# Performance work log

Hardware: AMD Instinct MI355X
Metric: run time of the kernel (lower is better)

Reference implementation:

```python
import jax, jax.numpy as jnp
import numpy as np

N_NODES = 40000
N_EDGES = 640000
D_IN, D_HID, D_OUT = 128, 128, 40


def _gcn_layer(x, src, dst, norm, W, b, n):
    # PyG GCNConv: h = x @ W; aggregate norm * h[src] at dst; add bias.
    h = x @ W
    msg = norm[:, None] * h[src]          # [E+N, d] gathered messages
    return jax.ops.segment_sum(msg, dst, num_segments=n) + b


def setup_inputs() -> dict:
    key = jax.random.key(0)
    ks = jax.random.split(key, 8)
    x = jax.random.normal(ks[0], (N_NODES, D_IN), dtype=jnp.float32)
    edge_index = jax.random.randint(ks[1], (2, N_EDGES), 0, N_NODES)
    s_in = 1.0 / np.sqrt(D_IN)
    s_hid = 1.0 / np.sqrt(D_HID)
    W1 = jax.random.normal(ks[2], (D_IN, D_HID), dtype=jnp.float32) * s_in
    b1 = jnp.zeros((D_HID,), dtype=jnp.float32)
    W2 = jax.random.normal(ks[3], (D_HID, D_HID), dtype=jnp.float32) * s_hid
    b2 = jnp.zeros((D_HID,), dtype=jnp.float32)
    W3 = jax.random.normal(ks[4], (D_HID, D_OUT), dtype=jnp.float32) * s_hid
    b3 = jnp.zeros((D_OUT,), dtype=jnp.float32)
    return {"x": x, "edge_index": edge_index, "W1": W1, "b1": b1,
            "W2": W2, "b2": b2, "W3": W3, "b3": b3}


def reference(x, edge_index, W1, b1, W2, b2, W3, b3):
    n = x.shape[0]
    src = edge_index[0].astype(jnp.int32)
    dst = edge_index[1].astype(jnp.int32)

    # --- GCN normalization with self-loops (PyG GCNConv defaults) ---
    loops = jnp.arange(n, dtype=jnp.int32)
    src2 = jnp.concatenate([src, loops])
    dst2 = jnp.concatenate([dst, loops])
    deg = jax.ops.segment_sum(jnp.ones_like(dst2, dtype=x.dtype), dst2,
                              num_segments=n)
    dis = jnp.where(deg > 0, jax.lax.rsqrt(deg), 0.0)
    norm = dis[src2] * dis[dst2]          # [E+N]

    h = jax.nn.relu(_gcn_layer(x, src2, dst2, norm, W1, b1, n))
    h = jax.nn.relu(_gcn_layer(h, src2, dst2, norm, W2, b2, n))
    out = _gcn_layer(h, src2, dst2, norm, W3, b3, n)

    # --- reg_loss = trace(A @ A), A = dense COO adjacency (dupes summed) ---
    # trace(A@A) = sum_{i,j} A[i,j] * A[j,i]
    #            = sum over edge instances (i,j) of multiplicity of (j,i).
    # Computed sparsely via sorted key lookup instead of NxN densification.
    keys = src * n + dst                  # unique int32 key per (i,j)
    skeys = jnp.sort(keys)
    rev = dst * n + src
    lo = jnp.searchsorted(skeys, rev, side="left")
    hi = jnp.searchsorted(skeys, rev, side="right")
    reg_loss = jnp.sum((hi - lo).astype(jnp.float32))

    return jax.nn.log_softmax(out, axis=1), reg_loss
```

## Files before the change

### kernel.cpp

```cpp
#include <hip/hip_runtime.h>
#include <hip/hip_bf16.h>
#include <math.h>

#define NN 40000
#define EE 640000
#define CAP 64
#define MPAD 40064
#define LDS_STRIDE 136
#define FP8_STRIDE 144
#define G_STRIDE 72
#define E4B 625

typedef short bf16x8 __attribute__((ext_vector_type(8)));
typedef float f32x16 __attribute__((ext_vector_type(16)));
typedef float f32x2 __attribute__((ext_vector_type(2)));

__device__ __forceinline__ unsigned bf16rne(float x) {
  unsigned u = __float_as_uint(x);
  return (u + 0x7fffu + ((u >> 16) & 1u)) >> 16;
}
__device__ __forceinline__ unsigned packbf2(float lo, float hi) {
  return bf16rne(lo) | (bf16rne(hi) << 16);
}
__device__ __forceinline__ float bflo(unsigned u) {
  return __uint_as_float(u << 16);
}
__device__ __forceinline__ float bfhi(unsigned u) {
  return __uint_as_float(u & 0xffff0000u);
}
__device__ __forceinline__ float dis_of(const int* cnt, int i) {
  return rsqrtf((float)(cnt[i] + 1));
}
__device__ __forceinline__ f32x2 cvt2lo(unsigned u) {
  return __builtin_amdgcn_cvt_pk_f32_fp8((int)u, false);
}
__device__ __forceinline__ f32x2 cvt2hi(unsigned u) {
  return __builtin_amdgcn_cvt_pk_f32_fp8((int)u, true);
}
__device__ __forceinline__ unsigned char f32_to_fp8(float x) {
  return (unsigned char)(__builtin_amdgcn_cvt_pk_fp8_f32(x, x, 0, false) & 0xff);
}

__global__ __launch_bounds__(256) void edge_w_kernel(
    const int4* __restrict__ src4, const int4* __restrict__ dst4,
    int* __restrict__ cnt, unsigned short* __restrict__ csr,
    const float* __restrict__ W1, const float* __restrict__ W2,
    const float* __restrict__ W3, unsigned short* __restrict__ Wt1,
    unsigned short* __restrict__ Wt2, unsigned short* __restrict__ W3t,
    unsigned* __restrict__ Xb32, unsigned* __restrict__ H1b32) {
  int blk = blockIdx.x, t = threadIdx.x;
  if (blk < E4B) {
    int e = blk * 256 + t;
    int4 s = src4[e];
    int4 d = dst4[e];
    int p0 = atomicAdd(&cnt[d.x], 1);
    int p1 = atomicAdd(&cnt[d.y], 1);
    int p2 = atomicAdd(&cnt[d.z], 1);
    int p3 = atomicAdd(&cnt[d.w], 1);
    if (p0 < CAP) csr[d.x * CAP + p0] = (unsigned short)s.x;
    if (p1 < CAP) csr[d.y * CAP + p1] = (unsigned short)s.y;
    if (p2 < CAP) csr[d.z * CAP + p2] = (unsigned short)s.z;
    if (p3 < CAP) csr[d.w * CAP + p3] = (unsigned short)s.w;
  } else if (blk < 753) {
    bool is1 = blk < 689;
    int n = (blk - (is1 ? 625 : 689)) * 2 + (t >> 7);
    int k = t & 127;
    const float* W = is1 ? W1 : W2;
    unsigned short* Wt = is1 ? Wt1 : Wt2;
    Wt[n * 128 + k] = (unsigned short)bf16rne(W[k * 128 + n]);
  } else if (blk < 785) {
    int n = (blk - 753) * 2 + (t >> 7);
    int k = t & 127;
    float v = (n < 40) ? W3[k * 40 + n] : 0.f;
    W3t[n * 128 + k] = (unsigned short)bf16rne(v);
  } else {
    if (t < 32) Xb32[(size_t)NN * 32 + t] = 0u;
    else if (t < 64) H1b32[(size_t)NN * 32 + (t - 32)] = 0u;
  }
}

__global__ __launch_bounds__(256) void fill_x_kernel(
    const int* __restrict__ cnt, const float4* __restrict__ X,
    uint2* __restrict__ Xb8v) {
  int i = blockIdx.x * 256 + threadIdx.x;
  float di = dis_of(cnt, i >> 4);
  float4 a = X[i * 2], b = X[i * 2 + 1];
  int lo = __builtin_amdgcn_cvt_pk_fp8_f32(di * a.x, di * a.y, 0, false);
  lo = __builtin_amdgcn_cvt_pk_fp8_f32(di * a.z, di * a.w, lo, true);
  int hi = __builtin_amdgcn_cvt_pk_fp8_f32(di * b.x, di * b.y, 0, false);
  hi = __builtin_amdgcn_cvt_pk_fp8_f32(di * b.z, di * b.w, hi, true);
  uint2 o;
  o.x = (unsigned)lo;
  o.y = (unsigned)hi;
  Xb8v[i] = o;
}

__device__ __forceinline__ void agg128_body8(
    int node, int sub, const unsigned char* __restrict__ Hb,
    const int* __restrict__ cnt, const unsigned short* __restrict__ csr,
    unsigned* __restrict__ outB) {
  float di = dis_of(cnt, node);
  const unsigned char* Hbs = Hb + sub * 16;
  f32x2 a0, a1, a2, a3, a4, a5, a6, a7;
  {
    uint4 v = *(const uint4*)&Hbs[(size_t)node * 128];
    a0 = cvt2lo(v.x);
    a1 = cvt2hi(v.x);
    a2 = cvt2lo(v.y);
    a3 = cvt2hi(v.y);
    a4 = cvt2lo(v.z);
    a5 = cvt2hi(v.z);
    a6 = cvt2lo(v.w);
    a7 = cvt2hi(v.w);
  }
  int cn = cnt[node];
  cn = cn > CAP ? CAP : cn;
  const unsigned short* row = &csr[node * CAP];
  if (cn > 0) {
    uint4 cs = *(const uint4*)row;
    for (int e = 0; e < cn; e += 8) {
      int rem = cn - e;
      int s0 = cs.x & 0xffff, s1 = cs.x >> 16;
      int s2 = cs.y & 0xffff, s3 = cs.y >> 16;
      int s4 = cs.z & 0xffff, s5 = cs.z >> 16;
      int s6 = cs.w & 0xffff, s7 = cs.w >> 16;
      s1 = rem > 1 ? s1 : NN;
      s2 = rem > 2 ? s2 : NN;
      s3 = rem > 3 ? s3 : NN;
      s4 = rem > 4 ? s4 : NN;
      s5 = rem > 5 ? s5 : NN;
      s6 = rem > 6 ? s6 : NN;
      s7 = rem > 7 ? s7 : NN;
      uint4 v0 = *(const uint4*)&Hbs[(size_t)s0 * 128];
      uint4 v1 = *(const uint4*)&Hbs[(size_t)s1 * 128];
      uint4 v2 = *(const uint4*)&Hbs[(size_t)s2 * 128];
      uint4 v3 = *(const uint4*)&Hbs[(size_t)s3 * 128];
      uint4 v4 = *(const uint4*)&Hbs[(size_t)s4 * 128];
      uint4 v5 = *(const uint4*)&Hbs[(size_t)s5 * 128];
      uint4 v6 = *(const uint4*)&Hbs[(size_t)s6 * 128];
      uint4 v7 = *(const uint4*)&Hbs[(size_t)s7 * 128];
      if (e + 8 < cn) cs = *(const uint4*)&row[e + 8];
#define ACC8(vv)                                    \
  a0 += cvt2lo(vv.x); a1 += cvt2hi(vv.x);           \
  a2 += cvt2lo(vv.y); a3 += cvt2hi(vv.y);           \
  a4 += cvt2lo(vv.z); a5 += cvt2hi(vv.z);           \
  a6 += cvt2lo(vv.w); a7 += cvt2hi(vv.w);
      ACC8(v0);
      ACC8(v1);
      ACC8(v2);
      ACC8(v3);
      ACC8(v4);
      ACC8(v5);
      ACC8(v6);
      ACC8(v7);
#undef ACC8
    }
  }
  unsigned o0 = packbf2(di * a0.x, di * a0.y);
  unsigned o1 = packbf2(di * a1.x, di * a1.y);
  unsigned o2 = packbf2(di * a2.x, di * a2.y);
  unsigned o3 = packbf2(di * a3.x, di * a3.y);
  unsigned o4 = packbf2(di * a4.x, di * a4.y);
  unsigned o5 = packbf2(di * a5.x, di * a5.y);
  unsigned o6 = packbf2(di * a6.x, di * a6.y);
  unsigned o7 = packbf2(di * a7.x, di * a7.y);
  *(uint4*)&outB[(size_t)node * 64 + sub * 8] = make_uint4(o0, o1, o2, o3);
  *(uint4*)&outB[(size_t)node * 64 + sub * 8 + 4] = make_uint4(o4, o5, o6, o7);
}

__global__ __launch_bounds__(256) void agg_reg(
    const unsigned char* __restrict__ Hb8, const int* __restrict__ cnt,
    const unsigned short* __restrict__ csr, unsigned* __restrict__ outB,
    const int* __restrict__ src, const int* __restrict__ dst, int ebase,
    float* __restrict__ out_scalar) {
  int blk = blockIdx.x, t = threadIdx.x;
  if ((blk & 1) == 0) {
    int node = (blk >> 1) * 32 + (t >> 3);
    agg128_body8(node, t & 7, Hb8, cnt, csr, outB);
    return;
  }
  int e = ebase + (blk >> 1) * 256 + t;
  int c = 0;
  {
    int i = src[e];
    unsigned j = (unsigned)dst[e];
    int cn = cnt[i];
    cn = cn > CAP ? CAP : cn;
    const uint4* base = (const uint4*)&csr[i * CAP];
    int full = cn >> 3;
    for (int q = 0; q < full; q++) {
      uint4 v = base[q];
      c += ((v.x & 0xffffu) == j) + ((v.x >> 16) == j);
      c += ((v.y & 0xffffu) == j) + ((v.y >> 16) == j);
      c += ((v.z & 0xffffu) == j) + ((v.z >> 16) == j);
      c += ((v.w & 0xffffu) == j) + ((v.w >> 16) == j);
    }
    int rem = cn & 7;
    if (rem) {
      uint4 v = base[full];
      c += (int)((v.x & 0xffffu) == j);
      c += ((v.x >> 16) == j) & (rem > 1);
      c += ((v.y & 0xffffu) == j) & (rem > 2);
      c += ((v.y >> 16) == j) & (rem > 3);
      c += ((v.z & 0xffffu) == j) & (rem > 4);
      c += ((v.z >> 16) == j) & (rem > 5);
      c += ((v.w & 0xffffu) == j) & (rem > 6);
    }
  }
  float v = (float)c;
  for (int off = 32; off; off >>= 1) v += __shfl_down(v, off, 64);
  __shared__ float ws[4];
  int lane = threadIdx.x & 63, w = threadIdx.x >> 6;
  if (lane == 0) ws[w] = v;
  __syncthreads();
  if (threadIdx.x == 0) atomicAdd(out_scalar, ws[0] + ws[1] + ws[2] + ws[3]);
}

__global__ __launch_bounds__(256) void gemm_mfma(
    const unsigned* __restrict__ Ab, const unsigned* __restrict__ Wt,
    const float* __restrict__ bias, const int* __restrict__ cnt,
    unsigned char* __restrict__ outB8) {
  __shared__ unsigned short At[128 * LDS_STRIDE];
  __shared__ unsigned short Bt[128 * LDS_STRIDE];
  __shared__ float dsh[128];
  int t = threadIdx.x;
  int rowBase = blockIdx.x * 128;
  if (t < 128) {
    int rr = rowBase + t;
    dsh[t] = (rr < NN) ? dis_of(cnt, rr) : 0.f;
  }
  {
    const uint4* ga = (const uint4*)(Ab + (size_t)rowBase * 64);
    const uint4* gw = (const uint4*)Wt;
#pragma unroll
    for (int i = 0; i < 8; i++) {
      int idx = i * 256 + t;
      int r = idx >> 4, c = idx & 15;
      uint4 va = ga[idx];
      uint4 vw = gw[idx];
      *(uint4*)&At[r * LDS_STRIDE + c * 8] = va;
      *(uint4*)&Bt[r * LDS_STRIDE + c * 8] = vw;
    }
  }
  __syncthreads();
  int lane = t & 63, w = t >> 6;
  int m31 = lane & 31;
  int khalf = (lane >> 5) * 8;
  f32x16 acc[4] = {};
#pragma unroll
  for (int ks = 0; ks < 8; ks++) {
    bf16x8 a = *(bf16x8*)&At[(w * 32 + m31) * LDS_STRIDE + ks * 16 + khalf];
#pragma unroll
    for (int nt = 0; nt < 4; nt++) {
      bf16x8 b = *(bf16x8*)&Bt[(nt * 32 + m31) * LDS_STRIDE + ks * 16 + khalf];
      acc[nt] = __builtin_amdgcn_mfma_f32_32x32x16_bf16(a, b, acc[nt], 0, 0, 0);
    }
  }
  __syncthreads();
  unsigned char* Ac = (unsigned char*)At;
  int rsel = (lane >> 5) * 4;
#pragma unroll
  for (int nt = 0; nt < 4; nt++) {
    int col = nt * 32 + m31;
    float bv = bias[col];
#pragma unroll
    for (int r = 0; r < 16; r++) {
      int rl = w * 32 + (r & 3) + 8 * (r >> 2) + rsel;
      float x = fmaxf(acc[nt][r] + bv, 0.f);
      Ac[rl * FP8_STRIDE + col] = f32_to_fp8(dsh[rl] * x);
    }
  }
  __syncthreads();
  {
#pragma unroll
    for (int i = 0; i < 4; i++) {
      int idx = i * 256 + t;
      int r = idx >> 3, c = idx & 7;
      int grow = rowBase + r;
      if (grow < NN) {
        uint4 vv = *(const uint4*)&Ac[r * FP8_STRIDE + c * 16];
        *(uint4*)&outB8[(size_t)grow * 128 + c * 16] = vv;
      }
    }
  }
}

__global__ __launch_bounds__(256) void gemm_mfma2(
    const unsigned* __restrict__ Ab, const unsigned* __restrict__ Wt,
    const float* __restrict__ bias, const int* __restrict__ cnt,
    const unsigned short* __restrict__ W3t, unsigned char* __restrict__ G3b) {
  __shared__ unsigned short At[128 * LDS_STRIDE];
  __shared__ unsigned short Bt[128 * LDS_STRIDE];
  __shared__ float dsh[128];
  int t = threadIdx.x;
  int rowBase = blockIdx.x * 128;
  if (blockIdx.x == 0 && t < 32)
    ((unsigned*)G3b)[(size_t)NN * 32 + t] = 0u;
  if (t < 128) {
    int rr = rowBase + t;
    dsh[t] = (rr < NN) ? dis_of(cnt, rr) : 0.f;
  }
  {
    const uint4* ga = (const uint4*)(Ab + (size_t)rowBase * 64);
    const uint4* gw = (const uint4*)Wt;
#pragma unroll
    for (int i = 0; i < 8; i++) {
      int idx = i * 256 + t;
      int r = idx >> 4, c = idx & 15;
      uint4 va = ga[idx];
      uint4 vw = gw[idx];
      *(uint4*)&At[r * LDS_STRIDE + c * 8] = va;
      *(uint4*)&Bt[r * LDS_STRIDE + c * 8] = vw;
    }
  }
  __syncthreads();
  int lane = t & 63, w = t >> 6;
  int m31 = lane & 31;
  int khalf = (lane >> 5) * 8;
  f32x16 acc[4] = {};
#pragma unroll
  for (int ks = 0; ks < 8; ks++) {
    bf16x8 a = *(bf16x8*)&At[(w * 32 + m31) * LDS_STRIDE + ks * 16 + khalf];
#pragma unroll
    for (int nt = 0; nt < 4; nt++) {
      bf16x8 b = *(bf16x8*)&Bt[(nt * 32 + m31) * LDS_STRIDE + ks * 16 + khalf];
      acc[nt] = __builtin_amdgcn_mfma_f32_32x32x16_bf16(a, b, acc[nt], 0, 0, 0);
    }
  }
  __syncthreads();
  int rsel = (lane >> 5) * 4;
#pragma unroll
  for (int nt = 0; nt < 4; nt++) {
    int col = nt * 32 + m31;
    float bv = bias[col];
#pragma unroll
    for (int r = 0; r < 16; r++) {
      int rl = w * 32 + (r & 3) + 8 * (r >> 2) + rsel;
      float x = fmaxf(acc[nt][r] + bv, 0.f);
      At[rl * LDS_STRIDE + col] = (unsigned short)bf16rne(dsh[rl] * x);
    }
  }
  {
    const uint4* gw3 = (const uint4*)W3t;
#pragma unroll
    for (int i = 0; i < 4; i++) {
      int idx = i * 256 + t;
      int r = idx >> 4, c = idx & 15;
      *(uint4*)&Bt[r * LDS_STRIDE + c * 8] = gw3[idx];
    }
  }
  __syncthreads();
  f32x16 acc2[2] = {};
#pragma unroll
  for (int ks = 0; ks < 8; ks++) {
    bf16x8 a = *(bf16x8*)&At[(w * 32 + m31) * LDS_STRIDE + ks * 16 + khalf];
#pragma unroll
    for (int nt = 0; nt < 2; nt++) {
      bf16x8 b = *(bf16x8*)&Bt[(nt * 32 + m31) * LDS_STRIDE + ks * 16 + khalf];
      acc2[nt] = __builtin_amdgcn_mfma_f32_32x32x16_bf16(a, b, acc2[nt], 0, 0, 0);
    }
  }
  __syncthreads();
  unsigned short* Gs = At;
#pragma unroll
  for (int nt = 0; nt < 2; nt++) {
    int col = nt * 32 + m31;
#pragma unroll
    for (int r = 0; r < 16; r++) {
      int rl = w * 32 + (r & 3) + 8 * (r >> 2) + rsel;
      Gs[rl * G_STRIDE + col] = (unsigned short)bf16rne(acc2[nt][r]);
    }
  }
  __syncthreads();
  {
#pragma unroll
    for (int i = 0; i < 4; i++) {
      int idx = i * 256 + t;
      int r = idx >> 3, c = idx & 7;
      int grow = rowBase + r;
      if (grow < NN) {
        uint4 vv = *(const uint4*)&Gs[r * G_STRIDE + c * 8];
        *(uint4*)&G3b[(size_t)grow * 128 + c * 16] = vv;
      }
    }
  }
}

__global__ __launch_bounds__(256) void agg40b_softmax(
    const unsigned char* __restrict__ Gb, const int* __restrict__ cnt,
    const unsigned short* __restrict__ csr, const float* __restrict__ b3,
    float* __restrict__ outp) {
  int t = threadIdx.x;
  int node = blockIdx.x * 32 + (t >> 3);
  int sub = t & 7;
  const unsigned char* Gs = Gb + sub * 16;
  float di = dis_of(cnt, node);
  float a0, a1, a2, a3, a4, a5, a6, a7;
  {
    uint4 v = *(const uint4*)&Gs[(size_t)node * 128];
    a0 = bflo(v.x); a1 = bfhi(v.x);
    a2 = bflo(v.y); a3 = bfhi(v.y);
    a4 = bflo(v.z); a5 = bfhi(v.z);
    a6 = bflo(v.w); a7 = bfhi(v.w);
  }
  int cn = cnt[node];
  cn = cn > CAP ? CAP : cn;
  const unsigned short* row = &csr[node * CAP];
  if (cn > 0) {
    uint4 cs = *(const uint4*)row;
    for (int e = 0; e < cn; e += 8) {
      int rem = cn - e;
      int s0 = cs.x & 0xffff, s1 = cs.x >> 16;
      int s2 = cs.y & 0xffff, s3 = cs.y >> 16;
      int s4 = cs.z & 0xffff, s5 = cs.z >> 16;
      int s6 = cs.w & 0xffff, s7 = cs.w >> 16;
      s1 = rem > 1 ? s1 : NN;
      s2 = rem > 2 ? s2 : NN;
      s3 = rem > 3 ? s3 : NN;
      s4 = rem > 4 ? s4 : NN;
      s5 = rem > 5 ? s5 : NN;
      s6 = rem > 6 ? s6 : NN;
      s7 = rem > 7 ? s7 : NN;
      uint4 v0 = *(const uint4*)&Gs[(size_t)s0 * 128];
      uint4 v1 = *(const uint4*)&Gs[(size_t)s1 * 128];
      uint4 v2 = *(const uint4*)&Gs[(size_t)s2 * 128];
      uint4 v3 = *(const uint4*)&Gs[(size_t)s3 * 128];
      uint4 v4 = *(const uint4*)&Gs[(size_t)s4 * 128];
      uint4 v5 = *(const uint4*)&Gs[(size_t)s5 * 128];
      uint4 v6 = *(const uint4*)&Gs[(size_t)s6 * 128];
      uint4 v7 = *(const uint4*)&Gs[(size_t)s7 * 128];
      if (e + 8 < cn) cs = *(const uint4*)&row[e + 8];
#define ACCB(vv)                                    \
  a0 += bflo(vv.x); a1 += bfhi(vv.x);               \
  a2 += bflo(vv.y); a3 += bfhi(vv.y);               \
  a4 += bflo(vv.z); a5 += bfhi(vv.z);               \
  a6 += bflo(vv.w); a7 += bfhi(vv.w);
      ACCB(v0);
      ACCB(v1);
      ACCB(v2);
      ACCB(v3);
      ACCB(v4);
      ACCB(v5);
      ACCB(v6);
      ACCB(v7);
#undef ACCB
    }
  }
  bool act = sub < 5;
  int sb = act ? sub : 0;
  const float4* b34 = (const float4*)b3;
  float4 bl = b34[sb * 2], bh = b34[sb * 2 + 1];
  float o0 = di * a0 + bl.x, o1 = di * a1 + bl.y;
  float o2 = di * a2 + bl.z, o3 = di * a3 + bl.w;
  float o4 = di * a4 + bh.x, o5 = di * a5 + bh.y;
  float o6 = di * a6 + bh.z, o7 = di * a7 + bh.w;
  float m = fmaxf(fmaxf(fmaxf(o0, o1), fmaxf(o2, o3)),
                  fmaxf(fmaxf(o4, o5), fmaxf(o6, o7)));
  m = act ? m : -1e30f;
  m = fmaxf(m, __shfl_xor(m, 1, 64));
  m = fmaxf(m, __shfl_xor(m, 2, 64));
  m = fmaxf(m, __shfl_xor(m, 4, 64));
  float s = expf(o0 - m) + expf(o1 - m) + expf(o2 - m) + expf(o3 - m) +
            expf(o4 - m) + expf(o5 - m) + expf(o6 - m) + expf(o7 - m);
  s = act ? s : 0.f;
  s += __shfl_xor(s, 1, 64);
  s += __shfl_xor(s, 2, 64);
  s += __shfl_xor(s, 4, 64);
  float l = m + logf(s);
  if (act) {
    float4 r0, r1;
    r0.x = o0 - l; r0.y = o1 - l; r0.z = o2 - l; r0.w = o3 - l;
    r1.x = o4 - l; r1.y = o5 - l; r1.z = o6 - l; r1.w = o7 - l;
    float* op = &outp[(size_t)node * 40 + sub * 8];
    *(float4*)op = r0;
    *(float4*)(op + 4) = r1;
  }
}

extern "C" void kernel_launch(void* const* d_in, const int* in_sizes, int n_in,
                              void* d_out, int out_size, void* d_ws,
                              size_t ws_size, hipStream_t stream) {
  const float* X = (const float*)d_in[0];
  const int* ei = (const int*)d_in[1];
  const float* W1 = (const float*)d_in[2];
  const float* b1 = (const float*)d_in[3];
  const float* W2 = (const float*)d_in[4];
  const float* b2 = (const float*)d_in[5];
  const float* W3 = (const float*)d_in[6];
  const float* b3 = (const float*)d_in[7];
  float* out = (float*)d_out;

  const int* src = ei;
  const int* dst = ei + EE;

  char* w = (char*)d_ws;
  auto carve = [&](size_t bytes) {
    char* p = w;
    w += (bytes + 255) & ~(size_t)255;
    return p;
  };
  int* cnt = (int*)carve(NN * 4);
  unsigned short* csr = (unsigned short*)carve((size_t)NN * CAP * 2);
  unsigned short* Wt1 = (unsigned short*)carve(128 * 128 * 2);
  unsigned short* Wt2 = (unsigned short*)carve(128 * 128 * 2);
  unsigned short* W3t = (unsigned short*)carve(64 * 128 * 2);
  unsigned* Ab = (unsigned*)carve((size_t)MPAD * 128 * 2);
  char* blk = carve(((size_t)NN + 1) * 128 * 2);
  unsigned char* Xb8 = (unsigned char*)blk;
  unsigned char* H1b8 = (unsigned char*)blk + ((size_t)NN + 1) * 128;
  unsigned char* G3b = (unsigned char*)blk;

  (void)hipMemsetAsync(cnt, 0, NN * 4, stream);
  (void)hipMemsetAsync((char*)d_out + (size_t)NN * 40 * 4, 0, 4, stream);

  const int GB = MPAD / 128;

  edge_w_kernel<<<786, 256, 0, stream>>>((const int4*)src, (const int4*)dst,
                                         cnt, csr, W1, W2, W3, Wt1, Wt2, W3t,
                                         (unsigned*)Xb8, (unsigned*)H1b8);
  fill_x_kernel<<<2500, 256, 0, stream>>>(cnt, (const float4*)X, (uint2*)Xb8);
  agg_reg<<<2500, 256, 0, stream>>>(Xb8, cnt, csr, Ab, src, dst, 0,
                                    out + (size_t)NN * 40);
  gemm_mfma<<<GB, 256, 0, stream>>>(Ab, (const unsigned*)Wt1, b1, cnt, H1b8);
  agg_reg<<<2500, 256, 0, stream>>>(H1b8, cnt, csr, Ab, src, dst, EE / 2,
                                    out + (size_t)NN * 40);
  gemm_mfma2<<<GB, 256, 0, stream>>>(Ab, (const unsigned*)Wt2, b2, cnt, W3t,
                                     G3b);
  agg40b_softmax<<<1250, 256, 0, stream>>>(G3b, cnt, csr, b3, out);
}
```

Before: 194.3 us.

## Split fp8 feature tables into halves and route aggregation work per XCC

Stores the fp8 node-feature tables as two 64-byte column halves, so each aggregation block gathers from only one half. Blocks pick their work through an atomic queue keyed on the XCC id, which steers each half toward a subset of XCDs and keeps its working set in that XCD's L2. CSR loads and bf16 output stores are made nontemporal. This adds per-block atomics and a shared-memory broadcast, and the XCC-to-half mapping depends on hardware dispatch order.

```diff
diff --git a/kernel.cpp b/kernel.cpp
--- a/kernel.cpp
+++ b/kernel.cpp
@@ -14,6 +14,8 @@
 typedef short bf16x8 __attribute__((ext_vector_type(8)));
 typedef float f32x16 __attribute__((ext_vector_type(16)));
 typedef float f32x2 __attribute__((ext_vector_type(2)));
+typedef unsigned u32x4 __attribute__((ext_vector_type(4)));
+typedef unsigned u32x2 __attribute__((ext_vector_type(2)));
 
 __device__ __forceinline__ unsigned bf16rne(float x) {
   unsigned u = __float_as_uint(x);
@@ -47,7 +49,8 @@
     const float* __restrict__ W1, const float* __restrict__ W2,
     const float* __restrict__ W3, unsigned short* __restrict__ Wt1,
     unsigned short* __restrict__ Wt2, unsigned short* __restrict__ W3t,
-    unsigned* __restrict__ Xb32, unsigned* __restrict__ H1b32) {
+    unsigned* __restrict__ XbA32, unsigned* __restrict__ XbB32,
+    unsigned* __restrict__ HA32, unsigned* __restrict__ HB32) {
   int blk = blockIdx.x, t = threadIdx.x;
   if (blk < E4B) {
     int e = blk * 256 + t;
@@ -74,16 +77,19 @@
     float v = (n < 40) ? W3[k * 40 + n] : 0.f;
     W3t[n * 128 + k] = (unsigned short)bf16rne(v);
   } else {
-    if (t < 32) Xb32[(size_t)NN * 32 + t] = 0u;
-    else if (t < 64) H1b32[(size_t)NN * 32 + (t - 32)] = 0u;
+    if (t < 16) XbA32[(size_t)NN * 16 + t] = 0u;
+    else if (t < 32) XbB32[(size_t)NN * 16 + (t - 16)] = 0u;
+    else if (t < 48) HA32[(size_t)NN * 16 + (t - 32)] = 0u;
+    else if (t < 64) HB32[(size_t)NN * 16 + (t - 48)] = 0u;
   }
 }
 
 __global__ __launch_bounds__(256) void fill_x_kernel(
     const int* __restrict__ cnt, const float4* __restrict__ X,
-    uint2* __restrict__ Xb8v) {
+    uint2* __restrict__ XbA2, uint2* __restrict__ XbB2) {
   int i = blockIdx.x * 256 + threadIdx.x;
-  float di = dis_of(cnt, i >> 4);
+  int row = i >> 4, li = i & 15;
+  float di = dis_of(cnt, row);
   float4 a = X[i * 2], b = X[i * 2 + 1];
   int lo = __builtin_amdgcn_cvt_pk_fp8_f32(di * a.x, di * a.y, 0, false);
   lo = __builtin_amdgcn_cvt_pk_fp8_f32(di * a.z, di * a.w, lo, true);
@@ -92,32 +98,29 @@
   uint2 o;
   o.x = (unsigned)lo;
   o.y = (unsigned)hi;
-  Xb8v[i] = o;
-}
-
-__device__ __forceinline__ void agg128_body8(
-    int node, int sub, const unsigned char* __restrict__ Hb,
+  if (li < 8) XbA2[row * 8 + li] = o;
+  else XbB2[row * 8 + (li - 8)] = o;
+}
+
+__device__ __forceinline__ void agg64_body(
+    int node, int sub, const unsigned char* __restrict__ T, int half,
     const int* __restrict__ cnt, const unsigned short* __restrict__ csr,
     unsigned* __restrict__ outB) {
   float di = dis_of(cnt, node);
-  const unsigned char* Hbs = Hb + sub * 16;
-  f32x2 a0, a1, a2, a3, a4, a5, a6, a7;
-  {
-    uint4 v = *(const uint4*)&Hbs[(size_t)node * 128];
+  const unsigned char* Hbs = T + sub * 8;
+  f32x2 a0, a1, a2, a3;
+  {
+    uint2 v = *(const uint2*)&Hbs[(size_t)node * 64];
     a0 = cvt2lo(v.x);
     a1 = cvt2hi(v.x);
     a2 = cvt2lo(v.y);
     a3 = cvt2hi(v.y);
-    a4 = cvt2lo(v.z);
-    a5 = cvt2hi(v.z);
-    a6 = cvt2lo(v.w);
-    a7 = cvt2hi(v.w);
   }
   int cn = cnt[node];
   cn = cn > CAP ? CAP : cn;
   const unsigned short* row = &csr[node * CAP];
   if (cn > 0) {
-    uint4 cs = *(const uint4*)row;
+    u32x4 cs = __builtin_nontemporal_load((const u32x4*)row);
     for (int e = 0; e < cn; e += 8) {
       int rem = cn - e;
       int s0 = cs.x & 0xffff, s1 = cs.x >> 16;
@@ -131,55 +134,72 @@
       s5 = rem > 5 ? s5 : NN;
       s6 = rem > 6 ? s6 : NN;
       s7 = rem > 7 ? s7 : NN;
-      uint4 v0 = *(const uint4*)&Hbs[(size_t)s0 * 128];
-      uint4 v1 = *(const uint4*)&Hbs[(size_t)s1 * 128];
-      uint4 v2 = *(const uint4*)&Hbs[(size_t)s2 * 128];
-      uint4 v3 = *(const uint4*)&Hbs[(size_t)s3 * 128];
-      uint4 v4 = *(const uint4*)&Hbs[(size_t)s4 * 128];
-      uint4 v5 = *(const uint4*)&Hbs[(size_t)s5 * 128];
-      uint4 v6 = *(const uint4*)&Hbs[(size_t)s6 * 128];
-      uint4 v7 = *(const uint4*)&Hbs[(size_t)s7 * 128];
-      if (e + 8 < cn) cs = *(const uint4*)&row[e + 8];
-#define ACC8(vv)                                    \
+      uint2 v0 = *(const uint2*)&Hbs[(size_t)s0 * 64];
+      uint2 v1 = *(const uint2*)&Hbs[(size_t)s1 * 64];
+      uint2 v2 = *(const uint2*)&Hbs[(size_t)s2 * 64];
+      uint2 v3 = *(const uint2*)&Hbs[(size_t)s3 * 64];
+      uint2 v4 = *(const uint2*)&Hbs[(size_t)s4 * 64];
+      uint2 v5 = *(const uint2*)&Hbs[(size_t)s5 * 64];
+      uint2 v6 = *(const uint2*)&Hbs[(size_t)s6 * 64];
+      uint2 v7 = *(const uint2*)&Hbs[(size_t)s7 * 64];
+      if (e + 8 < cn)
+        cs = __builtin_nontemporal_load((const u32x4*)&row[e + 8]);
+#define ACC2(vv)                                    \
   a0 += cvt2lo(vv.x); a1 += cvt2hi(vv.x);           \
-  a2 += cvt2lo(vv.y); a3 += cvt2hi(vv.y);           \
-  a4 += cvt2lo(vv.z); a5 += cvt2hi(vv.z);           \
-  a6 += cvt2lo(vv.w); a7 += cvt2hi(vv.w);
-      ACC8(v0);
-      ACC8(v1);
-      ACC8(v2);
-      ACC8(v3);
-      ACC8(v4);
-      ACC8(v5);
-      ACC8(v6);
-      ACC8(v7);
-#undef ACC8
-    }
-  }
-  unsigned o0 = packbf2(di * a0.x, di * a0.y);
-  unsigned o1 = packbf2(di * a1.x, di * a1.y);
-  unsigned o2 = packbf2(di * a2.x, di * a2.y);
-  unsigned o3 = packbf2(di * a3.x, di * a3.y);
-  unsigned o4 = packbf2(di * a4.x, di * a4.y);
-  unsigned o5 = packbf2(di * a5.x, di * a5.y);
-  unsigned o6 = packbf2(di * a6.x, di * a6.y);
-  unsigned o7 = packbf2(di * a7.x, di * a7.y);
-  *(uint4*)&outB[(size_t)node * 64 + sub * 8] = make_uint4(o0, o1, o2, o3);
-  *(uint4*)&outB[(size_t)node * 64 + sub * 8 + 4] = make_uint4(o4, o5, o6, o7);
+  a2 += cvt2lo(vv.y); a3 += cvt2hi(vv.y);
+      ACC2(v0);
+      ACC2(v1);
+      ACC2(v2);
+      ACC2(v3);
+      ACC2(v4);
+      ACC2(v5);
+      ACC2(v6);
+      ACC2(v7);
+#undef ACC2
+    }
+  }
+  u32x4 o;
+  o.x = packbf2(di * a0.x, di * a0.y);
+  o.y = packbf2(di * a1.x, di * a1.y);
+  o.z = packbf2(di * a2.x, di * a2.y);
+  o.w = packbf2(di * a3.x, di * a3.y);
+  __builtin_nontemporal_store(
+      o, (u32x4*)&outB[(size_t)node * 64 + half * 32 + sub * 4]);
 }
 
 __global__ __launch_bounds__(256) void agg_reg(
-    const unsigned char* __restrict__ Hb8, const int* __restrict__ cnt,
-    const unsigned short* __restrict__ csr, unsigned* __restrict__ outB,
-    const int* __restrict__ src, const int* __restrict__ dst, int ebase,
+    const unsigned char* __restrict__ TA, const unsigned char* __restrict__ TB,
+    const int* __restrict__ cnt, const unsigned short* __restrict__ csr,
+    unsigned* __restrict__ outB, const int* __restrict__ src,
+    const int* __restrict__ dst, int ebase, int* __restrict__ q,
     float* __restrict__ out_scalar) {
   int blk = blockIdx.x, t = threadIdx.x;
-  if ((blk & 1) == 0) {
-    int node = (blk >> 1) * 32 + (t >> 3);
-    agg128_body8(node, t & 7, Hb8, cnt, csr, outB);
+  bool isReg = (blk % 3 == 2) && (blk / 3 < 1250);
+  if (!isReg) {
+    __shared__ int job_s;
+    if (t == 0) {
+      unsigned xcc;
+      asm volatile("s_getreg_b32 %0, hwreg(HW_REG_XCC_ID)" : "=s"(xcc));
+      int h = (int)(xcc & 1u);
+      int w1 = atomicAdd(&q[h], 1);
+      int enc;
+      if (w1 < 1250) {
+        enc = (h << 16) | w1;
+      } else {
+        int w2 = atomicAdd(&q[h ^ 1], 1);
+        enc = (w2 < 1250) ? (((h ^ 1) << 16) | w2) : -1;
+      }
+      job_s = enc;
+    }
+    __syncthreads();
+    int enc = job_s;
+    if (enc < 0) return;
+    int half = enc >> 16, nb = enc & 0xffff;
+    int node = nb * 32 + (t >> 3);
+    agg64_body(node, t & 7, half ? TB : TA, half, cnt, csr, outB);
     return;
   }
-  int e = ebase + (blk >> 1) * 256 + t;
+  int e = ebase + (blk / 3) * 256 + t;
   int c = 0;
   {
     int i = src[e];
@@ -188,8 +208,8 @@
     cn = cn > CAP ? CAP : cn;
     const uint4* base = (const uint4*)&csr[i * CAP];
     int full = cn >> 3;
-    for (int q = 0; q < full; q++) {
-      uint4 v = base[q];
+    for (int qq = 0; qq < full; qq++) {
+      uint4 v = base[qq];
       c += ((v.x & 0xffffu) == j) + ((v.x >> 16) == j);
       c += ((v.y & 0xffffu) == j) + ((v.y >> 16) == j);
       c += ((v.z & 0xffffu) == j) + ((v.z >> 16) == j);
@@ -219,7 +239,7 @@
 __global__ __launch_bounds__(256) void gemm_mfma(
     const unsigned* __restrict__ Ab, const unsigned* __restrict__ Wt,
     const float* __restrict__ bias, const int* __restrict__ cnt,
-    unsigned char* __restrict__ outB8) {
+    unsigned char* __restrict__ HA8, unsigned char* __restrict__ HB8) {
   __shared__ unsigned short At[128 * LDS_STRIDE];
   __shared__ unsigned short Bt[128 * LDS_STRIDE];
   __shared__ float dsh[128];
@@ -279,7 +299,10 @@
       int grow = rowBase + r;
       if (grow < NN) {
         uint4 vv = *(const uint4*)&Ac[r * FP8_STRIDE + c * 16];
-        *(uint4*)&outB8[(size_t)grow * 128 + c * 16] = vv;
+        if (c < 4)
+          *(uint4*)&HA8[(size_t)grow * 64 + c * 16] = vv;
+        else
+          *(uint4*)&HB8[(size_t)grow * 64 + (c - 4) * 16] = vv;
       }
     }
   }
@@ -505,25 +528,31 @@
   unsigned short* Wt2 = (unsigned short*)carve(128 * 128 * 2);
   unsigned short* W3t = (unsigned short*)carve(64 * 128 * 2);
   unsigned* Ab = (unsigned*)carve((size_t)MPAD * 128 * 2);
-  char* blk = carve(((size_t)NN + 1) * 128 * 2);
-  unsigned char* Xb8 = (unsigned char*)blk;
-  unsigned char* H1b8 = (unsigned char*)blk + ((size_t)NN + 1) * 128;
+  const size_t HTB = ((size_t)NN + 1) * 64;
+  char* blk = carve(4 * HTB);
+  unsigned char* XbA = (unsigned char*)blk;
+  unsigned char* XbB = (unsigned char*)blk + HTB;
+  unsigned char* HA = (unsigned char*)blk + 2 * HTB;
+  unsigned char* HB = (unsigned char*)blk + 3 * HTB;
   unsigned char* G3b = (unsigned char*)blk;
+  int* qbuf = (int*)carve(16);
 
   (void)hipMemsetAsync(cnt, 0, NN * 4, stream);
+  (void)hipMemsetAsync(qbuf, 0, 16, stream);
   (void)hipMemsetAsync((char*)d_out + (size_t)NN * 40 * 4, 0, 4, stream);
 
   const int GB = MPAD / 128;
 
-  edge_w_kernel<<<786, 256, 0, stream>>>((const int4*)src, (const int4*)dst,
-                                         cnt, csr, W1, W2, W3, Wt1, Wt2, W3t,
-                                         (unsigned*)Xb8, (unsigned*)H1b8);
-  fill_x_kernel<<<2500, 256, 0, stream>>>(cnt, (const float4*)X, (uint2*)Xb8);
-  agg_reg<<<2500, 256, 0, stream>>>(Xb8, cnt, csr, Ab, src, dst, 0,
-                                    out + (size_t)NN * 40);
-  gemm_mfma<<<GB, 256, 0, stream>>>(Ab, (const unsigned*)Wt1, b1, cnt, H1b8);
-  agg_reg<<<2500, 256, 0, stream>>>(H1b8, cnt, csr, Ab, src, dst, EE / 2,
-                                    out + (size_t)NN * 40);
+  edge_w_kernel<<<786, 256, 0, stream>>>(
+      (const int4*)src, (const int4*)dst, cnt, csr, W1, W2, W3, Wt1, Wt2, W3t,
+      (unsigned*)XbA, (unsigned*)XbB, (unsigned*)HA, (unsigned*)HB);
+  fill_x_kernel<<<2500, 256, 0, stream>>>(cnt, (const float4*)X, (uint2*)XbA,
+                                          (uint2*)XbB);
+  agg_reg<<<3810, 256, 0, stream>>>(XbA, XbB, cnt, csr, Ab, src, dst, 0,
+                                    qbuf, out + (size_t)NN * 40);
+  gemm_mfma<<<GB, 256, 0, stream>>>(Ab, (const unsigned*)Wt1, b1, cnt, HA, HB);
+  agg_reg<<<3810, 256, 0, stream>>>(HA, HB, cnt, csr, Ab, src, dst, EE / 2,
+                                    qbuf + 2, out + (size_t)NN * 40);
   gemm_mfma2<<<GB, 256, 0, stream>>>(Ab, (const unsigned*)Wt2, b2, cnt, W3t,
                                      G3b);
   agg40b_softmax<<<1250, 256, 0, stream>>>(G3b, cnt, csr, b3, out);
```

Measured after the change: 238.6 us. +22.8%, slower.

## Spread reg-loss edge lookups across three aggregation kernels and de-vectorize CSR build

Applied to the files above, without the earlier changes.

The trace(A@A) lookup work is now split three ways instead of two, with the third share folded into the final aggregation/softmax kernel. Blocks are interleaved 3 aggregation to 2 reg blocks so the latency-bound edge scans overlap with the aggregation gathers. The CSR build now does one edge per thread instead of four, which raises parallelism for the atomics at the cost of more blocks. Partition sizes are 834+834+832 blocks of 256 edges, which together cover all edges.

```diff
diff --git a/kernel.cpp b/kernel.cpp
--- a/kernel.cpp
+++ b/kernel.cpp
@@ -9,7 +9,6 @@
 #define LDS_STRIDE 136
 #define FP8_STRIDE 144
 #define G_STRIDE 72
-#define E4B 625
 
 typedef short bf16x8 __attribute__((ext_vector_type(8)));
 typedef float f32x16 __attribute__((ext_vector_type(16)));
@@ -41,35 +40,70 @@
   return (unsigned char)(__builtin_amdgcn_cvt_pk_fp8_f32(x, x, 0, false) & 0xff);
 }
 
+__device__ __forceinline__ void reg_body(
+    int e, const int* __restrict__ src, const int* __restrict__ dst,
+    const int* __restrict__ cnt, const unsigned short* __restrict__ csr,
+    float* __restrict__ out_scalar) {
+  int t = threadIdx.x;
+  int c = 0;
+  {
+    int i = src[e];
+    unsigned j = (unsigned)dst[e];
+    int cn = cnt[i];
+    cn = cn > CAP ? CAP : cn;
+    const uint4* base = (const uint4*)&csr[i * CAP];
+    int full = cn >> 3;
+    for (int q = 0; q < full; q++) {
+      uint4 v = base[q];
+      c += ((v.x & 0xffffu) == j) + ((v.x >> 16) == j);
+      c += ((v.y & 0xffffu) == j) + ((v.y >> 16) == j);
+      c += ((v.z & 0xffffu) == j) + ((v.z >> 16) == j);
+      c += ((v.w & 0xffffu) == j) + ((v.w >> 16) == j);
+    }
+    int rem = cn & 7;
+    if (rem) {
+      uint4 v = base[full];
+      c += (int)((v.x & 0xffffu) == j);
+      c += ((v.x >> 16) == j) & (rem > 1);
+      c += ((v.y & 0xffffu) == j) & (rem > 2);
+      c += ((v.y >> 16) == j) & (rem > 3);
+      c += ((v.z & 0xffffu) == j) & (rem > 4);
+      c += ((v.z >> 16) == j) & (rem > 5);
+      c += ((v.w & 0xffffu) == j) & (rem > 6);
+    }
+  }
+  float v = (float)c;
+  for (int off = 32; off; off >>= 1) v += __shfl_down(v, off, 64);
+  __shared__ float ws[4];
+  int lane = t & 63, w = t >> 6;
+  if (lane == 0) ws[w] = v;
+  __syncthreads();
+  if (t == 0) atomicAdd(out_scalar, ws[0] + ws[1] + ws[2] + ws[3]);
+}
+
 __global__ __launch_bounds__(256) void edge_w_kernel(
-    const int4* __restrict__ src4, const int4* __restrict__ dst4,
+    const int* __restrict__ src, const int* __restrict__ dst,
     int* __restrict__ cnt, unsigned short* __restrict__ csr,
     const float* __restrict__ W1, const float* __restrict__ W2,
     const float* __restrict__ W3, unsigned short* __restrict__ Wt1,
     unsigned short* __restrict__ Wt2, unsigned short* __restrict__ W3t,
     unsigned* __restrict__ Xb32, unsigned* __restrict__ H1b32) {
   int blk = blockIdx.x, t = threadIdx.x;
-  if (blk < E4B) {
+  if (blk < 2500) {
     int e = blk * 256 + t;
-    int4 s = src4[e];
-    int4 d = dst4[e];
-    int p0 = atomicAdd(&cnt[d.x], 1);
-    int p1 = atomicAdd(&cnt[d.y], 1);
-    int p2 = atomicAdd(&cnt[d.z], 1);
-    int p3 = atomicAdd(&cnt[d.w], 1);
-    if (p0 < CAP) csr[d.x * CAP + p0] = (unsigned short)s.x;
-    if (p1 < CAP) csr[d.y * CAP + p1] = (unsigned short)s.y;
-    if (p2 < CAP) csr[d.z * CAP + p2] = (unsigned short)s.z;
-    if (p3 < CAP) csr[d.w * CAP + p3] = (unsigned short)s.w;
-  } else if (blk < 753) {
-    bool is1 = blk < 689;
-    int n = (blk - (is1 ? 625 : 689)) * 2 + (t >> 7);
+    int s = src[e];
+    int d = dst[e];
+    int p = atomicAdd(&cnt[d], 1);
+    if (p < CAP) csr[d * CAP + p] = (unsigned short)s;
+  } else if (blk < 2628) {
+    bool is1 = blk < 2564;
+    int n = (blk - (is1 ? 2500 : 2564)) * 2 + (t >> 7);
     int k = t & 127;
     const float* W = is1 ? W1 : W2;
     unsigned short* Wt = is1 ? Wt1 : Wt2;
     Wt[n * 128 + k] = (unsigned short)bf16rne(W[k * 128 + n]);
-  } else if (blk < 785) {
-    int n = (blk - 753) * 2 + (t >> 7);
+  } else if (blk < 2660) {
+    int n = (blk - 2628) * 2 + (t >> 7);
     int k = t & 127;
     float v = (n < 40) ? W3[k * 40 + n] : 0.f;
     W3t[n * 128 + k] = (unsigned short)bf16rne(v);
@@ -174,46 +208,17 @@
     const int* __restrict__ src, const int* __restrict__ dst, int ebase,
     float* __restrict__ out_scalar) {
   int blk = blockIdx.x, t = threadIdx.x;
-  if ((blk & 1) == 0) {
-    int node = (blk >> 1) * 32 + (t >> 3);
+  int g = blk / 5, r = blk % 5;
+  if (r < 3) {
+    int nb = g * 3 + r;
+    if (nb >= 1250) return;
+    int node = nb * 32 + (t >> 3);
     agg128_body8(node, t & 7, Hb8, cnt, csr, outB);
     return;
   }
-  int e = ebase + (blk >> 1) * 256 + t;
-  int c = 0;
-  {
-    int i = src[e];
-    unsigned j = (unsigned)dst[e];
-    int cn = cnt[i];
-    cn = cn > CAP ? CAP : cn;
-    const uint4* base = (const uint4*)&csr[i * CAP];
-    int full = cn >> 3;
-    for (int q = 0; q < full; q++) {
-      uint4 v = base[q];
-      c += ((v.x & 0xffffu) == j) + ((v.x >> 16) == j);
-      c += ((v.y & 0xffffu) == j) + ((v.y >> 16) == j);
-      c += ((v.z & 0xffffu) == j) + ((v.z >> 16) == j);
-      c += ((v.w & 0xffffu) == j) + ((v.w >> 16) == j);
-    }
-    int rem = cn & 7;
-    if (rem) {
-      uint4 v = base[full];
-      c += (int)((v.x & 0xffffu) == j);
-      c += ((v.x >> 16) == j) & (rem > 1);
-      c += ((v.y & 0xffffu) == j) & (rem > 2);
-      c += ((v.y >> 16) == j) & (rem > 3);
-      c += ((v.z & 0xffffu) == j) & (rem > 4);
-      c += ((v.z >> 16) == j) & (rem > 5);
-      c += ((v.w & 0xffffu) == j) & (rem > 6);
-    }
-  }
-  float v = (float)c;
-  for (int off = 32; off; off >>= 1) v += __shfl_down(v, off, 64);
-  __shared__ float ws[4];
-  int lane = threadIdx.x & 63, w = threadIdx.x >> 6;
-  if (lane == 0) ws[w] = v;
-  __syncthreads();
-  if (threadIdx.x == 0) atomicAdd(out_scalar, ws[0] + ws[1] + ws[2] + ws[3]);
+  int idx = g * 2 + (r - 3);
+  if (idx >= 834) return;
+  reg_body(ebase + idx * 256 + t, src, dst, cnt, csr, out_scalar);
 }
 
 __global__ __launch_bounds__(256) void gemm_mfma(
@@ -389,9 +394,19 @@
 __global__ __launch_bounds__(256) void agg40b_softmax(
     const unsigned char* __restrict__ Gb, const int* __restrict__ cnt,
     const unsigned short* __restrict__ csr, const float* __restrict__ b3,
-    float* __restrict__ outp) {
-  int t = threadIdx.x;
-  int node = blockIdx.x * 32 + (t >> 3);
+    float* __restrict__ outp, const int* __restrict__ src,
+    const int* __restrict__ dst, int ebase, float* __restrict__ out_scalar) {
+  int blk = blockIdx.x, t = threadIdx.x;
+  int g = blk / 5, r = blk % 5;
+  if (r >= 3) {
+    int idx = g * 2 + (r - 3);
+    if (idx < 832) reg_body(ebase + idx * 256 + t, src, dst, cnt, csr,
+                            out_scalar);
+    return;
+  }
+  int nb = g * 3 + r;
+  if (nb >= 1250) return;
+  int node = nb * 32 + (t >> 3);
   int sub = t & 7;
   const unsigned char* Gs = Gb + sub * 16;
   float di = dis_of(cnt, node);
@@ -515,16 +530,17 @@
 
   const int GB = MPAD / 128;
 
-  edge_w_kernel<<<786, 256, 0, stream>>>((const int4*)src, (const int4*)dst,
-                                         cnt, csr, W1, W2, W3, Wt1, Wt2, W3t,
-                                         (unsigned*)Xb8, (unsigned*)H1b8);
+  edge_w_kernel<<<2661, 256, 0, stream>>>(src, dst, cnt, csr, W1, W2, W3,
+                                          Wt1, Wt2, W3t, (unsigned*)Xb8,
+                                          (unsigned*)H1b8);
   fill_x_kernel<<<2500, 256, 0, stream>>>(cnt, (const float4*)X, (uint2*)Xb8);
-  agg_reg<<<2500, 256, 0, stream>>>(Xb8, cnt, csr, Ab, src, dst, 0,
+  agg_reg<<<2085, 256, 0, stream>>>(Xb8, cnt, csr, Ab, src, dst, 0,
                                     out + (size_t)NN * 40);
   gemm_mfma<<<GB, 256, 0, stream>>>(Ab, (const unsigned*)Wt1, b1, cnt, H1b8);
-  agg_reg<<<2500, 256, 0, stream>>>(H1b8, cnt, csr, Ab, src, dst, EE / 2,
+  agg_reg<<<2085, 256, 0, stream>>>(H1b8, cnt, csr, Ab, src, dst, 213504,
                                     out + (size_t)NN * 40);
   gemm_mfma2<<<GB, 256, 0, stream>>>(Ab, (const unsigned*)Wt2, b2, cnt, W3t,
                                      G3b);
-  agg40b_softmax<<<1250, 256, 0, stream>>>(G3b, cnt, csr, b3, out);
-}
+  agg40b_softmax<<<2085, 256, 0, stream>>>(G3b, cnt, csr, b3, out, src, dst,
+                                           427008, out + (size_t)NN * 40);
+}
```

Measured after the change: 194.8 us. Within noise of the previous version (+0.3%).
